# Kernel optimization log

Hardware: AMD Instinct MI355X
Metric: run time of the kernel (lower is better)

Reference implementation:

```python
import jax, jax.numpy as jnp
import numpy as np

VOL_RANGE = np.array([-40.0, -40.0, -1.0, 40.0, 40.0, 5.4], dtype=np.float32)
VOXEL = 0.8
NUM_CLASSES = 18
EMPTY_LABEL = NUM_CLASSES - 1
SCALE_MULT = 3.0
N_G = 1024
H, W, D = 100, 100, 8  # (vol_range[3:]-vol_range[:3]) / voxel_size


def quat_to_rotmat(q):
    # q: [N,4] (w,x,y,z), normalized here
    q = q / jnp.linalg.norm(q, axis=-1, keepdims=True)
    w, x, y, z = q[:, 0], q[:, 1], q[:, 2], q[:, 3]
    R = jnp.stack([
        1 - 2 * (y * y + z * z), 2 * (x * y - w * z), 2 * (x * z + w * y),
        2 * (x * y + w * z), 1 - 2 * (x * x + z * z), 2 * (y * z - w * x),
        2 * (x * z - w * y), 2 * (y * z + w * x), 1 - 2 * (x * x + y * y),
    ], axis=-1).reshape(-1, 3, 3)
    return R


def get_covariance(scales, R):
    M = R * scales[:, None, :]          # R @ diag(s)
    return jnp.einsum('nik,njk->nij', M, M)  # M M^T


def grid_points():
    lo = jnp.asarray(VOL_RANGE[:3])
    gx = (jnp.arange(H, dtype=jnp.float32) + 0.5) * VOXEL + lo[0]
    gy = (jnp.arange(W, dtype=jnp.float32) + 0.5) * VOXEL + lo[1]
    gz = (jnp.arange(D, dtype=jnp.float32) + 0.5) * VOXEL + lo[2]
    X, Y, Z = jnp.meshgrid(gx, gy, gz, indexing='ij')
    return jnp.stack([X, Y, Z], axis=-1).reshape(-1, 3)  # [P,3]


def setup_inputs() -> dict:
    key = jax.random.key(0)
    k1, k2, k3, k4, k5 = jax.random.split(key, 5)
    lo, hi = jnp.asarray(VOL_RANGE[:3]), jnp.asarray(VOL_RANGE[3:])
    means3d = jax.random.uniform(k1, (N_G, 3), minval=lo, maxval=hi)
    opacities = jax.random.uniform(k2, (N_G, 1))
    scales = jax.random.uniform(k3, (N_G, 3), minval=0.2, maxval=2.0)
    rotations = jax.random.normal(k4, (N_G, 4))
    features = jax.random.normal(k5, (N_G, NUM_CLASSES - 1))
    empty_scalar = jnp.ones((1,), jnp.float32) * 10.0
    return dict(means3d=means3d, opacities=opacities, scales=scales,
                rotations=rotations, features=features, empty_scalar=empty_scalar)


def reference(means3d, opacities, scales, rotations, features, empty_scalar):
    # covariances from scales + rotations (covariances=None path)
    cov = get_covariance(scales, quat_to_rotmat(rotations))  # [N,3,3]

    # append zero 'empty' channel, then append the empty background gaussian
    feats = jnp.concatenate([features, jnp.zeros_like(features[:, :1])], axis=-1)  # [N,C]
    empty_sem = jnp.zeros((1, NUM_CLASSES), jnp.float32).at[0, EMPTY_LABEL].add(empty_scalar[0])
    feats = jnp.concatenate([feats, empty_sem], axis=0)

    center = jnp.asarray((VOL_RANGE[:3] + VOL_RANGE[3:]) / 2.0)
    rng = jnp.abs(jnp.asarray(VOL_RANGE[:3] - VOL_RANGE[3:]))
    mu = jnp.concatenate([means3d, center[None]], axis=0)                 # [N+1,3]
    cov = jnp.concatenate([cov, jnp.diag(rng ** 2)[None]], axis=0)        # [N+1,3,3]
    opa = jnp.concatenate([opacities[:, 0], jnp.ones((1,))], axis=0)      # [N+1]
    sc = jnp.concatenate([scales, rng[None]], axis=0)                     # [N+1,3]

    x = grid_points()  # [P,3]

    # Mahalanobis distance via quadratic expansion (avoids [P,N,3] residuals):
    A = jnp.linalg.inv(cov)                        # [N+1,3,3]
    B = jnp.einsum('nij,nj->ni', A, mu)            # [N+1,3]
    c = jnp.einsum('ni,ni->n', B, mu)              # [N+1]
    xx = x[:, :, None] * x[:, None, :]             # [P,3,3]
    maha = jnp.einsum('pij,nij->pn', xx, A) - 2.0 * (x @ B.T) + c[None, :]  # [P,N+1]

    # local cutoff: |x - mu| <= scale_multiplier * scale per axis
    r = SCALE_MULT * sc  # [N+1,3]
    mask = jnp.ones((x.shape[0], mu.shape[0]), bool)
    for d in range(3):
        mask &= jnp.abs(x[:, d:d + 1] - mu[None, :, d]) <= r[None, :, d]

    w = jnp.where(mask, opa[None, :] * jnp.exp(-0.5 * maha), 0.0)  # [P,N+1]
    sem = w @ feats                                                # [P,C]

    grid_feats = sem.reshape(H, W, D, NUM_CLASSES)
    grid_density = jnp.zeros((H, W, D, 1), jnp.float32)
    return (grid_density, grid_feats)
```

## Files before the change

### kernel.cpp

```cpp
#include <hip/hip_runtime.h>

#define NG   1024
#define NCLS 18
#define HH   100
#define WW   100
#define DD   8
#define PTOT (HH*WW*DD)
#define TI   4
#define TJ   8
#define CH   128

__global__ __launch_bounds__(256) void gv_fused(
    const float* __restrict__ means, const float* __restrict__ opac,
    const float* __restrict__ scales, const float* __restrict__ rots,
    const float* __restrict__ feats, const float* __restrict__ es,
    float* __restrict__ out)
{
    __shared__ int   s_idx[NG];
    __shared__ float s_g[CH][32];
    __shared__ int   s_cnt;

    const int tid = threadIdx.x;
    const int i0  = blockIdx.x * TI;
    const int j0  = blockIdx.y * TJ;
    const int jmax = min(j0 + TJ - 1, WW - 1);

    const float xlo = (i0 + 0.5f) * 0.8f - 40.f;
    const float xhi = (i0 + TI - 1 + 0.5f) * 0.8f - 40.f;
    const float ylo = (j0 + 0.5f) * 0.8f - 40.f;
    const float yhi = (jmax + 0.5f) * 0.8f - 40.f;
    const float zlo = 0.5f * 0.8f - 1.f;
    const float zhi = (DD - 1 + 0.5f) * 0.8f - 1.f;

    if (tid == 0) s_cnt = 0;
    __syncthreads();

    #pragma unroll
    for (int n = tid; n < NG; n += 256) {
        float mx = means[n*3+0], my = means[n*3+1], mz = means[n*3+2];
        float rx = 3.f*scales[n*3+0], ry = 3.f*scales[n*3+1], rz = 3.f*scales[n*3+2];
        bool ov = (mx - rx <= xhi) & (mx + rx >= xlo)
                & (my - ry <= yhi) & (my + ry >= ylo)
                & (mz - rz <= zhi) & (mz + rz >= zlo);
        if (ov) s_idx[atomicAdd(&s_cnt, 1)] = n;
    }
    __syncthreads();
    const int ns = s_cnt;

    const int dk = tid & 7, dj = (tid >> 3) & 7, di = tid >> 6;
    const int i = i0 + di, j = j0 + dj, k = dk;
    const bool valid = (j < WW);
    const float x = (i + 0.5f) * 0.8f - 40.f;
    const float y = (j + 0.5f) * 0.8f - 40.f;
    const float z = (k + 0.5f) * 0.8f - 1.f;

    float acc[17];
    #pragma unroll
    for (int c = 0; c < 17; ++c) acc[c] = 0.f;

    for (int base = 0; base < ns; base += CH) {
        const int m = min(CH, ns - base);
        __syncthreads();
        if (tid < m) {
            int n = s_idx[base + tid];
            float qw = rots[n*4+0], qx = rots[n*4+1], qy = rots[n*4+2], qz = rots[n*4+3];
            float inv = rsqrtf(qw*qw + qx*qx + qy*qy + qz*qz);
            qw *= inv; qx *= inv; qy *= inv; qz *= inv;
            float R00 = 1.f - 2.f*(qy*qy + qz*qz), R01 = 2.f*(qx*qy - qw*qz), R02 = 2.f*(qx*qz + qw*qy);
            float R10 = 2.f*(qx*qy + qw*qz), R11 = 1.f - 2.f*(qx*qx + qz*qz), R12 = 2.f*(qy*qz - qw*qx);
            float R20 = 2.f*(qx*qz - qw*qy), R21 = 2.f*(qy*qz + qw*qx), R22 = 1.f - 2.f*(qx*qx + qy*qy);
            float sx = scales[n*3+0], sy = scales[n*3+1], sz = scales[n*3+2];
            float ix = 1.f/(sx*sx), iy = 1.f/(sy*sy), iz = 1.f/(sz*sz);
            float* g = s_g[tid];
            g[0] = means[n*3+0]; g[1] = means[n*3+1]; g[2] = means[n*3+2];
            g[3] = 3.f*sx; g[4] = 3.f*sy; g[5] = 3.f*sz;
            g[6]  = R00*R00*ix + R01*R01*iy + R02*R02*iz;
            g[7]  = R00*R10*ix + R01*R11*iy + R02*R12*iz;
            g[8]  = R00*R20*ix + R01*R21*iy + R02*R22*iz;
            g[9]  = R10*R10*ix + R11*R11*iy + R12*R12*iz;
            g[10] = R10*R20*ix + R11*R21*iy + R12*R22*iz;
            g[11] = R20*R20*ix + R21*R21*iy + R22*R22*iz;
            g[12] = opac[n];
            #pragma unroll
            for (int c = 0; c < 17; ++c) g[13+c] = feats[n*17+c];
        }
        __syncthreads();
        if (valid) {
            for (int t = 0; t < m; ++t) {
                const float* g = s_g[t];
                float dx = x - g[0], dy = y - g[1], dz = z - g[2];
                if (fabsf(dx) <= g[3] && fabsf(dy) <= g[4] && fabsf(dz) <= g[5]) {
                    float maha = dx*(dx*g[6] + 2.f*(dy*g[7] + dz*g[8]))
                               + dy*(dy*g[9] + 2.f*dz*g[10])
                               + dz*dz*g[11];
                    float w = g[12] * __expf(-0.5f * maha);
                    #pragma unroll
                    for (int c = 0; c < 17; ++c) acc[c] = fmaf(w, g[13+c], acc[c]);
                }
            }
        }
    }

    if (valid) {
        int p = (i*WW + j)*DD + k;
        float dz0 = z - 2.2f;
        float me  = x*x*(1.f/6400.f) + y*y*(1.f/6400.f) + dz0*dz0*(1.f/40.96f);
        float w17 = es[0] * __expf(-0.5f * me);
        out[p] = 0.f;
        float* o = out + PTOT + p*NCLS;
        #pragma unroll
        for (int c = 0; c < 17; ++c) o[c] = acc[c];
        o[17] = w17;
    }
}

extern "C" void kernel_launch(void* const* d_in, const int* in_sizes, int n_in,
                              void* d_out, int out_size, void* d_ws, size_t ws_size,
                              hipStream_t stream) {
    const float* means  = (const float*)d_in[0];
    const float* opac   = (const float*)d_in[1];
    const float* scales = (const float*)d_in[2];
    const float* rots   = (const float*)d_in[3];
    const float* feats  = (const float*)d_in[4];
    const float* es     = (const float*)d_in[5];
    float* out = (float*)d_out;

    dim3 grid((HH + TI - 1) / TI, (WW + TJ - 1) / TJ);
    gv_fused<<<grid, 256, 0, stream>>>(means, opac, scales, rots, feats, es, out);
}
```

Measured before the change: 74.85 us.

## Use single-wave 64-thread blocks with ballot compaction and float4 shared loads

Shrinks each block to one 64-lane wavefront covering a 2x4x8 voxel tile, so per-block gaussian culling is tighter and fewer gaussians pass the overlap test. The LDS atomic counter is replaced by wave ballot plus popcount prefix compaction, and the per-gaussian record is repacked so the inner loop reads it with float4 loads, fetching the covariance and feature words only when the cutoff test passes. The grid grows to 1250 blocks, each of which rescans all 1024 gaussians, so global reads in the culling phase rise.

```diff
diff --git a/kernel.cpp b/kernel.cpp
--- a/kernel.cpp
+++ b/kernel.cpp
@@ -6,50 +6,49 @@
 #define WW   100
 #define DD   8
 #define PTOT (HH*WW*DD)
-#define TI   4
-#define TJ   8
-#define CH   128
+#define TI   2
+#define TJ   4
+#define CH   64
 
-__global__ __launch_bounds__(256) void gv_fused(
+__global__ __launch_bounds__(64) void gv_fused(
     const float* __restrict__ means, const float* __restrict__ opac,
     const float* __restrict__ scales, const float* __restrict__ rots,
     const float* __restrict__ feats, const float* __restrict__ es,
     float* __restrict__ out)
 {
-    __shared__ int   s_idx[NG];
-    __shared__ float s_g[CH][32];
-    __shared__ int   s_cnt;
+    __shared__ int s_idx[NG];
+    __shared__ __align__(16) float s_g[CH][36];
 
     const int tid = threadIdx.x;
     const int i0  = blockIdx.x * TI;
     const int j0  = blockIdx.y * TJ;
-    const int jmax = min(j0 + TJ - 1, WW - 1);
 
     const float xlo = (i0 + 0.5f) * 0.8f - 40.f;
-    const float xhi = (i0 + TI - 1 + 0.5f) * 0.8f - 40.f;
+    const float xhi = (i0 + TI - 0.5f) * 0.8f - 40.f;
     const float ylo = (j0 + 0.5f) * 0.8f - 40.f;
-    const float yhi = (jmax + 0.5f) * 0.8f - 40.f;
-    const float zlo = 0.5f * 0.8f - 1.f;
-    const float zhi = (DD - 1 + 0.5f) * 0.8f - 1.f;
+    const float yhi = (j0 + TJ - 0.5f) * 0.8f - 40.f;
+    const float zlo = -0.6f, zhi = 5.0f;
 
-    if (tid == 0) s_cnt = 0;
-    __syncthreads();
-
-    #pragma unroll
-    for (int n = tid; n < NG; n += 256) {
+    int ns = 0;
+    #pragma unroll 4
+    for (int it = 0; it < NG / 64; ++it) {
+        int n = it * 64 + tid;
         float mx = means[n*3+0], my = means[n*3+1], mz = means[n*3+2];
         float rx = 3.f*scales[n*3+0], ry = 3.f*scales[n*3+1], rz = 3.f*scales[n*3+2];
         bool ov = (mx - rx <= xhi) & (mx + rx >= xlo)
                 & (my - ry <= yhi) & (my + ry >= ylo)
                 & (mz - rz <= zhi) & (mz + rz >= zlo);
-        if (ov) s_idx[atomicAdd(&s_cnt, 1)] = n;
+        unsigned long long m = __ballot(ov);
+        if (ov) {
+            int pos = __popcll(m & ((1ull << tid) - 1ull));
+            s_idx[ns + pos] = n;
+        }
+        ns += (int)__popcll(m);
     }
     __syncthreads();
-    const int ns = s_cnt;
 
-    const int dk = tid & 7, dj = (tid >> 3) & 7, di = tid >> 6;
-    const int i = i0 + di, j = j0 + dj, k = dk;
-    const bool valid = (j < WW);
+    const int k = tid & 7, dj = (tid >> 3) & 3, di = tid >> 5;
+    const int i = i0 + di, j = j0 + dj;
     const float x = (i + 0.5f) * 0.8f - 40.f;
     const float y = (j + 0.5f) * 0.8f - 40.f;
     const float z = (k + 0.5f) * 0.8f - 1.f;
@@ -72,46 +71,53 @@
             float sx = scales[n*3+0], sy = scales[n*3+1], sz = scales[n*3+2];
             float ix = 1.f/(sx*sx), iy = 1.f/(sy*sy), iz = 1.f/(sz*sz);
             float* g = s_g[tid];
-            g[0] = means[n*3+0]; g[1] = means[n*3+1]; g[2] = means[n*3+2];
-            g[3] = 3.f*sx; g[4] = 3.f*sy; g[5] = 3.f*sz;
-            g[6]  = R00*R00*ix + R01*R01*iy + R02*R02*iz;
-            g[7]  = R00*R10*ix + R01*R11*iy + R02*R12*iz;
-            g[8]  = R00*R20*ix + R01*R21*iy + R02*R22*iz;
-            g[9]  = R10*R10*ix + R11*R11*iy + R12*R12*iz;
-            g[10] = R10*R20*ix + R11*R21*iy + R12*R22*iz;
-            g[11] = R20*R20*ix + R21*R21*iy + R22*R22*iz;
-            g[12] = opac[n];
+            g[0] = means[n*3+0]; g[1] = means[n*3+1]; g[2] = means[n*3+2]; g[3] = 3.f*sx;
+            g[4] = 3.f*sy; g[5] = 3.f*sz; g[6] = opac[n];
+            g[7]  = R00*R00*ix + R01*R01*iy + R02*R02*iz;
+            g[8]  = R00*R10*ix + R01*R11*iy + R02*R12*iz;
+            g[9]  = R00*R20*ix + R01*R21*iy + R02*R22*iz;
+            g[10] = R10*R10*ix + R11*R11*iy + R12*R12*iz;
+            g[11] = R10*R20*ix + R11*R21*iy + R12*R22*iz;
+            g[12] = R20*R20*ix + R21*R21*iy + R22*R22*iz;
             #pragma unroll
-            for (int c = 0; c < 17; ++c) g[13+c] = feats[n*17+c];
+            for (int c = 0; c < 17; ++c) g[13 + c] = feats[n*17 + c];
+            g[30] = 0.f; g[31] = 0.f;
         }
         __syncthreads();
-        if (valid) {
-            for (int t = 0; t < m; ++t) {
-                const float* g = s_g[t];
-                float dx = x - g[0], dy = y - g[1], dz = z - g[2];
-                if (fabsf(dx) <= g[3] && fabsf(dy) <= g[4] && fabsf(dz) <= g[5]) {
-                    float maha = dx*(dx*g[6] + 2.f*(dy*g[7] + dz*g[8]))
-                               + dy*(dy*g[9] + 2.f*dz*g[10])
-                               + dz*dz*g[11];
-                    float w = g[12] * __expf(-0.5f * maha);
-                    #pragma unroll
-                    for (int c = 0; c < 17; ++c) acc[c] = fmaf(w, g[13+c], acc[c]);
-                }
+
+        for (int t = 0; t < m; ++t) {
+            const float4* gq = (const float4*)s_g[t];
+            float4 q0 = gq[0], q1 = gq[1];
+            float dx = x - q0.x, dy = y - q0.y, dz = z - q0.z;
+            if (fabsf(dx) <= q0.w && fabsf(dy) <= q1.x && fabsf(dz) <= q1.y) {
+                float4 q2 = gq[2], q3 = gq[3];
+                float maha = dx*(dx*q1.w + 2.f*(dy*q2.x + dz*q2.y))
+                           + dy*(dy*q2.z + 2.f*dz*q2.w)
+                           + dz*dz*q3.x;
+                float w = q1.z * __expf(-0.5f * maha);
+                float4 q4 = gq[4], q5 = gq[5], q6 = gq[6], q7 = gq[7];
+                acc[0]  = fmaf(w, q3.y, acc[0]);  acc[1]  = fmaf(w, q3.z, acc[1]);
+                acc[2]  = fmaf(w, q3.w, acc[2]);
+                acc[3]  = fmaf(w, q4.x, acc[3]);  acc[4]  = fmaf(w, q4.y, acc[4]);
+                acc[5]  = fmaf(w, q4.z, acc[5]);  acc[6]  = fmaf(w, q4.w, acc[6]);
+                acc[7]  = fmaf(w, q5.x, acc[7]);  acc[8]  = fmaf(w, q5.y, acc[8]);
+                acc[9]  = fmaf(w, q5.z, acc[9]);  acc[10] = fmaf(w, q5.w, acc[10]);
+                acc[11] = fmaf(w, q6.x, acc[11]); acc[12] = fmaf(w, q6.y, acc[12]);
+                acc[13] = fmaf(w, q6.z, acc[13]); acc[14] = fmaf(w, q6.w, acc[14]);
+                acc[15] = fmaf(w, q7.x, acc[15]); acc[16] = fmaf(w, q7.y, acc[16]);
             }
         }
     }
 
-    if (valid) {
-        int p = (i*WW + j)*DD + k;
-        float dz0 = z - 2.2f;
-        float me  = x*x*(1.f/6400.f) + y*y*(1.f/6400.f) + dz0*dz0*(1.f/40.96f);
-        float w17 = es[0] * __expf(-0.5f * me);
-        out[p] = 0.f;
-        float* o = out + PTOT + p*NCLS;
-        #pragma unroll
-        for (int c = 0; c < 17; ++c) o[c] = acc[c];
-        o[17] = w17;
-    }
+    const int p = (i * WW + j) * DD + k;
+    float dz0 = z - 2.2f;
+    float me  = x*x*(1.f/6400.f) + y*y*(1.f/6400.f) + dz0*dz0*(1.f/40.96f);
+    float w17 = es[0] * __expf(-0.5f * me);
+    out[p] = 0.f;
+    float* o = out + PTOT + p * NCLS;
+    #pragma unroll
+    for (int c = 0; c < 17; ++c) o[c] = acc[c];
+    o[17] = w17;
 }
 
 extern "C" void kernel_launch(void* const* d_in, const int* in_sizes, int n_in,
@@ -125,6 +131,6 @@
     const float* es     = (const float*)d_in[5];
     float* out = (float*)d_out;
 
-    dim3 grid((HH + TI - 1) / TI, (WW + TJ - 1) / TJ);
-    gv_fused<<<grid, 256, 0, stream>>>(means, opac, scales, rots, feats, es, out);
+    dim3 grid(HH / TI, WW / TJ);
+    gv_fused<<<grid, 64, 0, stream>>>(means, opac, scales, rots, feats, es, out);
 }
```

New measurement: 75.25 us. Within noise of the previous version (+0.5%).
